# Optimization experiments

Hardware: AMD Instinct MI355X
Metric: run time of the kernel (lower is better)

Reference implementation:

```python
import math
import jax, jax.numpy as jnp
import numpy as np

B, L, D = 2, 2048, 1024
NH = 16
HS = D // NH
BLOCK_SIZE = 2048


def setup_inputs() -> dict:
    key = jax.random.key(0)
    ks = jax.random.split(key, 4)
    x = jax.random.normal(ks[0], (B, L, D), dtype=jnp.float32)
    Wqkv = jax.random.normal(ks[1], (D, 3 * D), dtype=jnp.float32) * 0.02
    bqkv = jnp.zeros((3 * D,), dtype=jnp.float32)
    Wproj = jax.random.normal(ks[2], (D, D), dtype=jnp.float32) * 0.02
    bproj = jnp.zeros((D,), dtype=jnp.float32)
    Er = jax.random.normal(ks[3], (BLOCK_SIZE, HS), dtype=jnp.float32)
    return {"x": x, "Wqkv": Wqkv, "bqkv": bqkv, "Wproj": Wproj, "bproj": bproj, "Er": Er}


def _skew(QEr):
    # QEr: [B, nh, L, L]  (Music Transformer skew trick)
    b, nh, nr, nc = QEr.shape
    padded = jnp.pad(QEr, ((0, 0), (0, 0), (0, 0), (1, 0)))  # [B, nh, nr, nc+1]
    reshaped = padded.reshape(b, nh, nc + 1, nr)
    return reshaped[:, :, 1:, :]  # [B, nh, nr, nc]


def reference(x, Wqkv, bqkv, Wproj, bproj, Er):
    b, l, d = x.shape
    qkv = x @ Wqkv + bqkv  # [B, L, 3D]
    q, k, v = jnp.split(qkv, 3, axis=2)
    q = q.reshape(b, l, NH, HS).transpose(0, 2, 1, 3)  # [B, nh, L, hs]
    k = k.reshape(b, l, NH, HS).transpose(0, 2, 1, 3)
    v = v.reshape(b, l, NH, HS).transpose(0, 2, 1, 3)

    start = BLOCK_SIZE - l
    Er_t = Er[start:, :].T  # [hs, L]
    QEr = jnp.einsum('bhld,dm->bhlm', q, Er_t)  # [B, nh, L, L]
    Srel = _skew(QEr)

    QK_t = jnp.einsum('bhld,bhmd->bhlm', q, k)
    scale = 1.0 / math.sqrt(HS)
    att = (QK_t + Srel) * scale
    causal = jnp.tril(jnp.ones((l, l), dtype=bool))
    att = jnp.where(causal[None, None, :, :], att, jnp.float32(-jnp.inf))
    att = jax.nn.softmax(att, axis=-1)
    y = jnp.einsum('bhlm,bhmd->bhld', att, v)
    y = y.transpose(0, 2, 1, 3).reshape(b, l, d)
    return y @ Wproj + bproj
```

## Files before the change

kernel.cpp:

```cpp
#include <hip/hip_runtime.h>
#include <stdint.h>

#define BB 2
#define LL 2048
#define DD 1024
#define NHH 16
#define HSS 64

typedef __bf16 bf16x8 __attribute__((ext_vector_type(8)));
typedef float f32x4 __attribute__((ext_vector_type(4)));

__device__ __forceinline__ bf16x8 load8(const float* p) {
  float4 f0 = *(const float4*)p;
  float4 f1 = *(const float4*)(p + 4);
  bf16x8 v;
  v[0] = (__bf16)f0.x; v[1] = (__bf16)f0.y; v[2] = (__bf16)f0.z; v[3] = (__bf16)f0.w;
  v[4] = (__bf16)f1.x; v[5] = (__bf16)f1.y; v[6] = (__bf16)f1.z; v[7] = (__bf16)f1.w;
  return v;
}
__device__ __forceinline__ bf16x8 load8(const __bf16* p) {
  return *(const bf16x8*)p;
}

__device__ __forceinline__ void async_ld16(__bf16* lds_uniform_base,
                                           const __bf16* gptr_per_lane) {
  __builtin_amdgcn_global_load_lds(
      (const __attribute__((address_space(1))) void*)gptr_per_lane,
      (__attribute__((address_space(3))) void*)lds_uniform_base, 16, 0, 0);
}

__global__ void prep_k(const float* __restrict__ Wqkv, const float* __restrict__ x,
                       __bf16* __restrict__ WqkvT, __bf16* __restrict__ xb) {
  __shared__ __bf16 tile[32][33];
  int tx = threadIdx.x, ty = threadIdx.y;
  if (blockIdx.z == 1) {
    if (blockIdx.x >= 2048) return;
    int tid = ty * 32 + tx;
    size_t off = ((size_t)blockIdx.x * 256 + tid) * 8;
    *(bf16x8*)&xb[off] = load8(&x[off]);
    return;
  }
  int c0 = (blockIdx.x % 96) * 32, r0 = (blockIdx.x / 96) * 32;
#pragma unroll
  for (int i = ty; i < 32; i += 8)
    tile[i][tx] = (__bf16)Wqkv[(size_t)(r0 + i) * 3072 + c0 + tx];
  __syncthreads();
#pragma unroll
  for (int i = ty; i < 32; i += 8)
    WqkvT[(size_t)(c0 + i) * 1024 + r0 + tx] = tile[tx][i];
}

__global__ void tconv_k(const float* __restrict__ src, __bf16* __restrict__ dst,
                        int R, int C) {
  __shared__ __bf16 tile[32][33];
  int c0 = blockIdx.x * 32, r0 = blockIdx.y * 32;
  int tx = threadIdx.x, ty = threadIdx.y;
#pragma unroll
  for (int i = ty; i < 32; i += 8)
    tile[i][tx] = (__bf16)src[(size_t)(r0 + i) * C + c0 + tx];
  __syncthreads();
#pragma unroll
  for (int i = ty; i < 32; i += 8)
    dst[(size_t)(c0 + i) * R + r0 + tx] = tile[tx][i];
}

__global__ void vtrans_k(const __bf16* __restrict__ src, __bf16* __restrict__ dst) {
  __shared__ __bf16 tile[32][33];
  int bh = blockIdx.z;
  int l0 = blockIdx.x * 32, d0 = blockIdx.y * 32;
  const __bf16* s = src + (size_t)bh * LL * HSS;
  __bf16* d = dst + (size_t)bh * HSS * LL;
  int tx = threadIdx.x, ty = threadIdx.y;
#pragma unroll
  for (int i = ty; i < 32; i += 8)
    tile[i][tx] = s[(size_t)(l0 + i) * HSS + d0 + tx];
  __syncthreads();
#pragma unroll
  for (int i = ty; i < 32; i += 8)
    d[(size_t)(d0 + i) * LL + l0 + tx] = tile[tx][i];
}

template <int NTILE>
__global__ __launch_bounds__(256) void gemm_async_k(
    const __bf16* __restrict__ A, const __bf16* __restrict__ Bt,
    const float* __restrict__ bias, int M, int N, int K, int mode,
    float* __restrict__ out, __bf16* __restrict__ Qo,
    __bf16* __restrict__ Ko, __bf16* __restrict__ Vo) {
  constexpr int NF = NTILE / 32;
  constexpr int BG = NTILE / 64;
  __shared__ __align__(16) __bf16 As[128 * 32];
  __shared__ __align__(16) __bf16 Bs[NTILE * 32];
  int t = threadIdx.x;
  int wave = t >> 6, lane = t & 63, qd = lane >> 4, lr = lane & 15;
  int m0 = blockIdx.y * 128, n0 = blockIdx.x * NTILE;
  int wm = (wave >> 1) * 64, wn = (wave & 1) * (NTILE / 2);
  f32x4 acc[4][NF] = {};
  int srow = lane >> 2, sch = (lane & 3) * 8;

  const __bf16* Ab[2];
  const __bf16* Bb[BG];
#pragma unroll
  for (int c = 0; c < 2; c++)
    Ab[c] = A + (size_t)(m0 + (wave * 2 + c) * 16 + srow) * K + sch;
#pragma unroll
  for (int c = 0; c < BG; c++)
    Bb[c] = Bt + (size_t)(n0 + (wave * BG + c) * 16 + srow) * K + sch;

  for (int k0 = 0; k0 < K; k0 += 32) {
    __syncthreads();
#pragma unroll
    for (int c = 0; c < 2; c++)
      async_ld16(&As[(wave * 2 + c) * 512], Ab[c] + k0);
#pragma unroll
    for (int c = 0; c < BG; c++)
      async_ld16(&Bs[(wave * BG + c) * 512], Bb[c] + k0);
    __syncthreads();
    bf16x8 af[4], bfr[NF];
#pragma unroll
    for (int mt = 0; mt < 4; mt++)
      af[mt] = *(const bf16x8*)&As[(wm + mt * 16 + lr) * 32 + qd * 8];
#pragma unroll
    for (int nt = 0; nt < NF; nt++)
      bfr[nt] = *(const bf16x8*)&Bs[(wn + nt * 16 + lr) * 32 + qd * 8];
#pragma unroll
    for (int mt = 0; mt < 4; mt++)
#pragma unroll
      for (int nt = 0; nt < NF; nt++)
        acc[mt][nt] = __builtin_amdgcn_mfma_f32_16x16x32_bf16(af[mt], bfr[nt],
                                                              acc[mt][nt], 0, 0, 0);
  }
  float bvv[NF];
#pragma unroll
  for (int nt = 0; nt < NF; nt++) bvv[nt] = bias[n0 + wn + nt * 16 + lr];
#pragma unroll
  for (int mt = 0; mt < 4; mt++) {
#pragma unroll
    for (int nt = 0; nt < NF; nt++) {
#pragma unroll
      for (int r = 0; r < 4; r++) {
        int row = m0 + wm + mt * 16 + qd * 4 + r;
        int col = n0 + wn + nt * 16 + lr;
        float v = acc[mt][nt][r] + bvv[nt];
        if (mode == 1) {
          out[(size_t)row * N + col] = v;
        } else {
          __bf16 bb = (__bf16)v;
          int b = row >> 11, l = row & 2047;
          int h = (col >> 6) & 15, d = col & 63;
          __bf16* dst = (col < DD) ? Qo : (col < 2 * DD) ? Ko : Vo;
          dst[(((size_t)(b * NHH + h)) * LL + l) * HSS + d] = bb;
        }
      }
    }
  }
}

__global__ __launch_bounds__(256, 2) void flash_k(
    const __bf16* __restrict__ Qg, const __bf16* __restrict__ Kg,
    const __bf16* __restrict__ Vtg, const float* __restrict__ Erg,
    __bf16* __restrict__ Yg) {
  __shared__ __align__(16) __bf16 Kld[64 * 72];
  __shared__ __align__(16) __bf16 Vld[80 * 72];
  __shared__ __align__(16) __bf16 Erld[128 * 72];
  __shared__ __align__(16) __bf16 Pball[4][16 * 72];

  int bh = blockIdx.y;
  const __bf16* Qh = Qg + (size_t)bh * LL * HSS;
  const __bf16* Kh = Kg + (size_t)bh * LL * HSS;
  const __bf16* Vth = Vtg + (size_t)bh * HSS * LL;
  int b = bh >> 4, h = bh & 15;
  int t = threadIdx.x, wave = t >> 6, lane = t & 63, qd = lane >> 4, lr = lane & 15;
  __bf16* Pb = &Pball[wave][0];
  int cbase = 48 - wave * 16;

  for (int idx = t; idx < 16 * 72; idx += 256) {
    int rr = idx / 72;
    Vld[(64 + rr) * 72 + (idx - rr * 72)] = (rr == 0) ? (__bf16)1.f : (__bf16)0.f;
  }

  int jj = t >> 2, hf = t & 3;
  int er = t >> 1, ec = (t & 1) * 32;

#pragma unroll 1
  for (int pass = 0; pass < 2; pass++) {
    int tile = (pass == 0) ? (int)blockIdx.x : (31 - (int)blockIdx.x);
    int i0 = tile * 64;

    bf16x8 aq[2];
    {
      const __bf16* qrow = Qh + (size_t)(i0 + wave * 16 + lr) * HSS + qd * 8;
      aq[0] = *(const bf16x8*)qrow;
      aq[1] = *(const bf16x8*)(qrow + 32);
    }
    f32x4 oacc[5] = {};

    bf16x8 kr0, kr1, vr0, vr1, ergs[4];
    auto prefetch = [&](int j0) {
      kr0 = *(const bf16x8*)&Kh[(size_t)(j0 + jj) * HSS + hf * 16];
      kr1 = *(const bf16x8*)&Kh[(size_t)(j0 + jj) * HSS + hf * 16 + 8];
      vr0 = *(const bf16x8*)&Vth[(size_t)jj * LL + j0 + hf * 16];
      vr1 = *(const bf16x8*)&Vth[(size_t)jj * LL + j0 + hf * 16 + 8];
      int e = LL - 64 - i0 + j0 + er;
      if (e < LL) {
#pragma unroll
        for (int kx = 0; kx < 4; kx++)
          ergs[kx] = load8(&Erg[(size_t)e * HSS + ec + kx * 8]);
      } else {
        bf16x8 z;
#pragma unroll
        for (int q = 0; q < 8; q++) z[q] = (__bf16)0.f;
#pragma unroll
        for (int kx = 0; kx < 4; kx++) ergs[kx] = z;
      }
    };
    prefetch(0);

    for (int j0 = 0; j0 <= i0; j0 += 64) {
      __syncthreads();
      *(bf16x8*)&Kld[jj * 72 + hf * 16] = kr0;
      *(bf16x8*)&Kld[jj * 72 + hf * 16 + 8] = kr1;
      *(bf16x8*)&Vld[jj * 72 + hf * 16] = vr0;
      *(bf16x8*)&Vld[jj * 72 + hf * 16 + 8] = vr1;
#pragma unroll
      for (int kx = 0; kx < 4; kx++)
        *(bf16x8*)&Erld[er * 72 + ec + kx * 8] = ergs[kx];
      __syncthreads();
      if (j0 + 64 <= i0) prefetch(j0 + 64);

      f32x4 sacc[4] = {};
#pragma unroll
      for (int ct = 0; ct < 4; ct++)
#pragma unroll
        for (int kc = 0; kc < 2; kc++) {
          bf16x8 bk = *(const bf16x8*)&Kld[(ct * 16 + lr) * 72 + kc * 32 + qd * 8];
          sacc[ct] = __builtin_amdgcn_mfma_f32_16x16x32_bf16(aq[kc], bk, sacc[ct], 0, 0, 0);
        }
      f32x4 racc[5] = {};
#pragma unroll
      for (int ct = 0; ct < 5; ct++)
#pragma unroll
        for (int kc = 0; kc < 2; kc++) {
          bf16x8 be = *(const bf16x8*)&Erld[(cbase + ct * 16 + lr) * 72 + kc * 32 + qd * 8];
          racc[ct] = __builtin_amdgcn_mfma_f32_16x16x32_bf16(aq[kc], be, racc[ct], 0, 0, 0);
        }

#pragma unroll
      for (int r = 0; r < 4; r++) {
        int tr = qd * 4 + r;
        int base = 15 - tr + lr;
        int src = qd * 16 + (base & 15);
        int hi = base >> 4;
        float sh[5];
#pragma unroll
        for (int ct = 0; ct < 5; ct++) sh[ct] = __shfl(racc[ct][r], src, 64);
        int gi = i0 + wave * 16 + tr;
#pragma unroll
        for (int ct2 = 0; ct2 < 4; ct2++) {
          float rel = hi ? sh[ct2 + 1] : sh[ct2];
          float s = (sacc[ct2][r] + rel) * 0.125f;
          int gj = j0 + ct2 * 16 + lr;
          float p = (gj <= gi) ? __expf(s) : 0.f;
          Pb[tr * 72 + ct2 * 16 + lr] = (__bf16)p;
        }
      }

      bf16x8 ap0 = *(const bf16x8*)&Pb[lr * 72 + qd * 8];
      bf16x8 ap1 = *(const bf16x8*)&Pb[lr * 72 + 32 + qd * 8];
#pragma unroll
      for (int dt = 0; dt < 5; dt++) {
        bf16x8 bv0 = *(const bf16x8*)&Vld[(dt * 16 + lr) * 72 + qd * 8];
        bf16x8 bv1 = *(const bf16x8*)&Vld[(dt * 16 + lr) * 72 + 32 + qd * 8];
        oacc[dt] = __builtin_amdgcn_mfma_f32_16x16x32_bf16(ap0, bv0, oacc[dt], 0, 0, 0);
        oacc[dt] = __builtin_amdgcn_mfma_f32_16x16x32_bf16(ap1, bv1, oacc[dt], 0, 0, 0);
      }
    }

#pragma unroll
    for (int r = 0; r < 4; r++) {
      float lv = __shfl(oacc[4][r], qd * 16, 64);
      float inv = 1.f / lv;
      int l = i0 + wave * 16 + qd * 4 + r;
#pragma unroll
      for (int dt = 0; dt < 4; dt++) {
        int d = dt * 16 + lr;
        Yg[((size_t)(b * LL) + l) * DD + h * HSS + d] = (__bf16)(oacc[dt][r] * inv);
      }
    }
  }
}

extern "C" void kernel_launch(void* const* d_in, const int* in_sizes, int n_in,
                              void* d_out, int out_size, void* d_ws, size_t ws_size,
                              hipStream_t stream) {
  const float* x = (const float*)d_in[0];
  const float* Wqkv = (const float*)d_in[1];
  const float* bqkv = (const float*)d_in[2];
  const float* Wproj = (const float*)d_in[3];
  const float* bproj = (const float*)d_in[4];
  const float* Er = (const float*)d_in[5];
  float* out = (float*)d_out;

  if (ws_size < 4u * 8388608u) return;

  uint8_t* w = (uint8_t*)d_ws;
  __bf16* Q = (__bf16*)w;  w += (size_t)BB * NHH * LL * HSS * 2;
  __bf16* Kt = (__bf16*)w; w += (size_t)BB * NHH * LL * HSS * 2;
  __bf16* Vt = (__bf16*)w; w += (size_t)BB * NHH * LL * HSS * 2;
  __bf16* Y = (__bf16*)w;  w += (size_t)BB * LL * DD * 2;

  __bf16* xb = Y;
  __bf16* WqkvT = (__bf16*)d_out;
  __bf16* Vtmp = (__bf16*)((uint8_t*)d_out + (size_t)3072 * 1024 * 2);
  __bf16* WprojT = Q;

  prep_k<<<dim3(3072, 1, 2), dim3(32, 8), 0, stream>>>(Wqkv, x, WqkvT, xb);
  gemm_async_k<128><<<dim3(3072 / 128, 4096 / 128), 256, 0, stream>>>(
      xb, WqkvT, bqkv, 4096, 3072, 1024, 0, nullptr, Q, Kt, Vtmp);
  vtrans_k<<<dim3(LL / 32, HSS / 32, BB * NHH), dim3(32, 8), 0, stream>>>(Vtmp, Vt);
  flash_k<<<dim3(16, BB * NHH), 256, 0, stream>>>(Q, Kt, Vt, Er, Y);
  tconv_k<<<dim3(1024 / 32, 1024 / 32), dim3(32, 8), 0, stream>>>(Wproj, WprojT, 1024, 1024);
  gemm_async_k<64><<<dim3(1024 / 64, 4096 / 128), 256, 0, stream>>>(
      Y, WprojT, bproj, 4096, 1024, 1024, 1, out, nullptr, nullptr, nullptr);
}
```

Before: 259.9 us.

## Fuse transposes into GEMMs, pre-convert Er, and split flash tiles per block

The QKV GEMM epilogue now writes V directly in transposed layout, which removes the separate vtrans kernel. The projection GEMM reads fp32 Wproj and transposes it into LDS itself, which removes the tconv kernel. Er is converted to bf16 once in the prep kernel, and flash reads its fragments straight from global memory instead of staging them in LDS. Flash now runs one query tile per block (grid 32x32, largest tiles first, occupancy hint 3) instead of pairing tiles over two passes. This cuts launches and LDS use, but adds strided V stores, an uncoalesced Er gather from global, and a scalar LDS transpose in the projection GEMM.

```diff
diff --git a/kernel.cpp b/kernel.cpp
--- a/kernel.cpp
+++ b/kernel.cpp
@@ -30,16 +30,23 @@
 }
 
 __global__ void prep_k(const float* __restrict__ Wqkv, const float* __restrict__ x,
-                       __bf16* __restrict__ WqkvT, __bf16* __restrict__ xb) {
-  __shared__ __bf16 tile[32][33];
+                       const float* __restrict__ Er, __bf16* __restrict__ WqkvT,
+                       __bf16* __restrict__ xb, __bf16* __restrict__ Erb) {
   int tx = threadIdx.x, ty = threadIdx.y;
+  int tid = ty * 32 + tx;
   if (blockIdx.z == 1) {
     if (blockIdx.x >= 2048) return;
-    int tid = ty * 32 + tx;
     size_t off = ((size_t)blockIdx.x * 256 + tid) * 8;
     *(bf16x8*)&xb[off] = load8(&x[off]);
     return;
   }
+  if (blockIdx.z == 2) {
+    if (blockIdx.x >= 64) return;
+    size_t off = ((size_t)blockIdx.x * 256 + tid) * 8;
+    *(bf16x8*)&Erb[off] = load8(&Er[off]);
+    return;
+  }
+  __shared__ __bf16 tile[32][33];
   int c0 = (blockIdx.x % 96) * 32, r0 = (blockIdx.x / 96) * 32;
 #pragma unroll
   for (int i = ty; i < 32; i += 8)
@@ -50,121 +57,139 @@
     WqkvT[(size_t)(c0 + i) * 1024 + r0 + tx] = tile[tx][i];
 }
 
-__global__ void tconv_k(const float* __restrict__ src, __bf16* __restrict__ dst,
-                        int R, int C) {
-  __shared__ __bf16 tile[32][33];
-  int c0 = blockIdx.x * 32, r0 = blockIdx.y * 32;
-  int tx = threadIdx.x, ty = threadIdx.y;
-#pragma unroll
-  for (int i = ty; i < 32; i += 8)
-    tile[i][tx] = (__bf16)src[(size_t)(r0 + i) * C + c0 + tx];
-  __syncthreads();
-#pragma unroll
-  for (int i = ty; i < 32; i += 8)
-    dst[(size_t)(c0 + i) * R + r0 + tx] = tile[tx][i];
-}
-
-__global__ void vtrans_k(const __bf16* __restrict__ src, __bf16* __restrict__ dst) {
-  __shared__ __bf16 tile[32][33];
-  int bh = blockIdx.z;
-  int l0 = blockIdx.x * 32, d0 = blockIdx.y * 32;
-  const __bf16* s = src + (size_t)bh * LL * HSS;
-  __bf16* d = dst + (size_t)bh * HSS * LL;
-  int tx = threadIdx.x, ty = threadIdx.y;
-#pragma unroll
-  for (int i = ty; i < 32; i += 8)
-    tile[i][tx] = s[(size_t)(l0 + i) * HSS + d0 + tx];
-  __syncthreads();
-#pragma unroll
-  for (int i = ty; i < 32; i += 8)
-    d[(size_t)(d0 + i) * LL + l0 + tx] = tile[tx][i];
-}
-
-template <int NTILE>
-__global__ __launch_bounds__(256) void gemm_async_k(
+__global__ __launch_bounds__(256) void gemm_qkv_k(
     const __bf16* __restrict__ A, const __bf16* __restrict__ Bt,
-    const float* __restrict__ bias, int M, int N, int K, int mode,
-    float* __restrict__ out, __bf16* __restrict__ Qo,
-    __bf16* __restrict__ Ko, __bf16* __restrict__ Vo) {
-  constexpr int NF = NTILE / 32;
-  constexpr int BG = NTILE / 64;
+    const float* __restrict__ bias, __bf16* __restrict__ Qo,
+    __bf16* __restrict__ Ko, __bf16* __restrict__ Vto) {
+  const int K = 1024;
   __shared__ __align__(16) __bf16 As[128 * 32];
-  __shared__ __align__(16) __bf16 Bs[NTILE * 32];
+  __shared__ __align__(16) __bf16 Bs[128 * 32];
   int t = threadIdx.x;
   int wave = t >> 6, lane = t & 63, qd = lane >> 4, lr = lane & 15;
-  int m0 = blockIdx.y * 128, n0 = blockIdx.x * NTILE;
-  int wm = (wave >> 1) * 64, wn = (wave & 1) * (NTILE / 2);
-  f32x4 acc[4][NF] = {};
+  int m0 = blockIdx.y * 128, n0 = blockIdx.x * 128;
+  int wm = (wave >> 1) * 64, wn = (wave & 1) * 64;
+  f32x4 acc[4][4] = {};
   int srow = lane >> 2, sch = (lane & 3) * 8;
-
   const __bf16* Ab[2];
-  const __bf16* Bb[BG];
-#pragma unroll
-  for (int c = 0; c < 2; c++)
+  const __bf16* Bb[2];
+#pragma unroll
+  for (int c = 0; c < 2; c++) {
     Ab[c] = A + (size_t)(m0 + (wave * 2 + c) * 16 + srow) * K + sch;
-#pragma unroll
-  for (int c = 0; c < BG; c++)
-    Bb[c] = Bt + (size_t)(n0 + (wave * BG + c) * 16 + srow) * K + sch;
-
+    Bb[c] = Bt + (size_t)(n0 + (wave * 2 + c) * 16 + srow) * K + sch;
+  }
   for (int k0 = 0; k0 < K; k0 += 32) {
     __syncthreads();
 #pragma unroll
-    for (int c = 0; c < 2; c++)
+    for (int c = 0; c < 2; c++) {
       async_ld16(&As[(wave * 2 + c) * 512], Ab[c] + k0);
-#pragma unroll
-    for (int c = 0; c < BG; c++)
-      async_ld16(&Bs[(wave * BG + c) * 512], Bb[c] + k0);
-    __syncthreads();
-    bf16x8 af[4], bfr[NF];
+      async_ld16(&Bs[(wave * 2 + c) * 512], Bb[c] + k0);
+    }
+    __syncthreads();
+    bf16x8 af[4], bfr[4];
 #pragma unroll
     for (int mt = 0; mt < 4; mt++)
       af[mt] = *(const bf16x8*)&As[(wm + mt * 16 + lr) * 32 + qd * 8];
 #pragma unroll
-    for (int nt = 0; nt < NF; nt++)
+    for (int nt = 0; nt < 4; nt++)
       bfr[nt] = *(const bf16x8*)&Bs[(wn + nt * 16 + lr) * 32 + qd * 8];
 #pragma unroll
     for (int mt = 0; mt < 4; mt++)
 #pragma unroll
-      for (int nt = 0; nt < NF; nt++)
+      for (int nt = 0; nt < 4; nt++)
         acc[mt][nt] = __builtin_amdgcn_mfma_f32_16x16x32_bf16(af[mt], bfr[nt],
                                                               acc[mt][nt], 0, 0, 0);
   }
-  float bvv[NF];
-#pragma unroll
-  for (int nt = 0; nt < NF; nt++) bvv[nt] = bias[n0 + wn + nt * 16 + lr];
-#pragma unroll
-  for (int mt = 0; mt < 4; mt++) {
-#pragma unroll
-    for (int nt = 0; nt < NF; nt++) {
+  float bvv[4];
+#pragma unroll
+  for (int nt = 0; nt < 4; nt++) bvv[nt] = bias[n0 + wn + nt * 16 + lr];
+#pragma unroll
+  for (int mt = 0; mt < 4; mt++)
+#pragma unroll
+    for (int nt = 0; nt < 4; nt++)
 #pragma unroll
       for (int r = 0; r < 4; r++) {
         int row = m0 + wm + mt * 16 + qd * 4 + r;
         int col = n0 + wn + nt * 16 + lr;
-        float v = acc[mt][nt][r] + bvv[nt];
-        if (mode == 1) {
-          out[(size_t)row * N + col] = v;
+        __bf16 bb = (__bf16)(acc[mt][nt][r] + bvv[nt]);
+        int b = row >> 11, l = row & 2047;
+        int h = (col >> 6) & 15, d = col & 63;
+        if (col < DD) {
+          Qo[(((size_t)(b * NHH + h)) * LL + l) * HSS + d] = bb;
+        } else if (col < 2 * DD) {
+          Ko[(((size_t)(b * NHH + h)) * LL + l) * HSS + d] = bb;
         } else {
-          __bf16 bb = (__bf16)v;
-          int b = row >> 11, l = row & 2047;
-          int h = (col >> 6) & 15, d = col & 63;
-          __bf16* dst = (col < DD) ? Qo : (col < 2 * DD) ? Ko : Vo;
-          dst[(((size_t)(b * NHH + h)) * LL + l) * HSS + d] = bb;
+          Vto[(((size_t)(b * NHH + h)) * HSS + d) * LL + l] = bb;
         }
       }
-    }
-  }
-}
-
-__global__ __launch_bounds__(256, 2) void flash_k(
+}
+
+__global__ __launch_bounds__(256) void gemm_proj_k(
+    const __bf16* __restrict__ A, const float* __restrict__ Bg,
+    const float* __restrict__ bias, float* __restrict__ out) {
+  const int K = 1024, N = 1024;
+  __shared__ __align__(16) __bf16 As[128 * 32];
+  __shared__ __align__(16) __bf16 Bs[64 * 40];
+  int t = threadIdx.x;
+  int wave = t >> 6, lane = t & 63, qd = lane >> 4, lr = lane & 15;
+  int m0 = blockIdx.y * 128, n0 = blockIdx.x * 64;
+  int wm = (wave >> 1) * 64, wn = (wave & 1) * 32;
+  f32x4 acc[4][2] = {};
+  int srow = lane >> 2, sch = (lane & 3) * 8;
+  const __bf16* Ab[2];
+#pragma unroll
+  for (int c = 0; c < 2; c++)
+    Ab[c] = A + (size_t)(m0 + (wave * 2 + c) * 16 + srow) * K + sch;
+  int kk = t >> 3, nn = (t & 7) * 8;
+  const float* Bp = Bg + (size_t)kk * N + n0 + nn;
+
+  for (int k0 = 0; k0 < K; k0 += 32) {
+    __syncthreads();
+#pragma unroll
+    for (int c = 0; c < 2; c++)
+      async_ld16(&As[(wave * 2 + c) * 512], Ab[c] + k0);
+    bf16x8 bv = load8(Bp + (size_t)k0 * N);
+#pragma unroll
+    for (int j = 0; j < 8; j++) Bs[(nn + j) * 40 + kk] = bv[j];
+    __syncthreads();
+    bf16x8 af[4], bfr[2];
+#pragma unroll
+    for (int mt = 0; mt < 4; mt++)
+      af[mt] = *(const bf16x8*)&As[(wm + mt * 16 + lr) * 32 + qd * 8];
+#pragma unroll
+    for (int nt = 0; nt < 2; nt++)
+      bfr[nt] = *(const bf16x8*)&Bs[(wn + nt * 16 + lr) * 40 + qd * 8];
+#pragma unroll
+    for (int mt = 0; mt < 4; mt++)
+#pragma unroll
+      for (int nt = 0; nt < 2; nt++)
+        acc[mt][nt] = __builtin_amdgcn_mfma_f32_16x16x32_bf16(af[mt], bfr[nt],
+                                                              acc[mt][nt], 0, 0, 0);
+  }
+  float bvv[2];
+#pragma unroll
+  for (int nt = 0; nt < 2; nt++) bvv[nt] = bias[n0 + wn + nt * 16 + lr];
+#pragma unroll
+  for (int mt = 0; mt < 4; mt++)
+#pragma unroll
+    for (int nt = 0; nt < 2; nt++)
+#pragma unroll
+      for (int r = 0; r < 4; r++) {
+        int row = m0 + wm + mt * 16 + qd * 4 + r;
+        int col = n0 + wn + nt * 16 + lr;
+        out[(size_t)row * N + col] = acc[mt][nt][r] + bvv[nt];
+      }
+}
+
+__global__ __launch_bounds__(256, 3) void flash_k(
     const __bf16* __restrict__ Qg, const __bf16* __restrict__ Kg,
-    const __bf16* __restrict__ Vtg, const float* __restrict__ Erg,
+    const __bf16* __restrict__ Vtg, const __bf16* __restrict__ Erb,
     __bf16* __restrict__ Yg) {
   __shared__ __align__(16) __bf16 Kld[64 * 72];
   __shared__ __align__(16) __bf16 Vld[80 * 72];
-  __shared__ __align__(16) __bf16 Erld[128 * 72];
   __shared__ __align__(16) __bf16 Pball[4][16 * 72];
 
-  int bh = blockIdx.y;
+  int bh = blockIdx.x;
+  int i0 = (31 - (int)blockIdx.y) * 64;
   const __bf16* Qh = Qg + (size_t)bh * LL * HSS;
   const __bf16* Kh = Kg + (size_t)bh * LL * HSS;
   const __bf16* Vth = Vtg + (size_t)bh * HSS * LL;
@@ -179,112 +204,100 @@
   }
 
   int jj = t >> 2, hf = t & 3;
-  int er = t >> 1, ec = (t & 1) * 32;
-
-#pragma unroll 1
-  for (int pass = 0; pass < 2; pass++) {
-    int tile = (pass == 0) ? (int)blockIdx.x : (31 - (int)blockIdx.x);
-    int i0 = tile * 64;
-
-    bf16x8 aq[2];
-    {
-      const __bf16* qrow = Qh + (size_t)(i0 + wave * 16 + lr) * HSS + qd * 8;
-      aq[0] = *(const bf16x8*)qrow;
-      aq[1] = *(const bf16x8*)(qrow + 32);
-    }
-    f32x4 oacc[5] = {};
-
-    bf16x8 kr0, kr1, vr0, vr1, ergs[4];
-    auto prefetch = [&](int j0) {
-      kr0 = *(const bf16x8*)&Kh[(size_t)(j0 + jj) * HSS + hf * 16];
-      kr1 = *(const bf16x8*)&Kh[(size_t)(j0 + jj) * HSS + hf * 16 + 8];
-      vr0 = *(const bf16x8*)&Vth[(size_t)jj * LL + j0 + hf * 16];
-      vr1 = *(const bf16x8*)&Vth[(size_t)jj * LL + j0 + hf * 16 + 8];
-      int e = LL - 64 - i0 + j0 + er;
-      if (e < LL) {
-#pragma unroll
-        for (int kx = 0; kx < 4; kx++)
-          ergs[kx] = load8(&Erg[(size_t)e * HSS + ec + kx * 8]);
-      } else {
-        bf16x8 z;
-#pragma unroll
-        for (int q = 0; q < 8; q++) z[q] = (__bf16)0.f;
-#pragma unroll
-        for (int kx = 0; kx < 4; kx++) ergs[kx] = z;
+
+  bf16x8 aq[2];
+  {
+    const __bf16* qrow = Qh + (size_t)(i0 + wave * 16 + lr) * HSS + qd * 8;
+    aq[0] = *(const bf16x8*)qrow;
+    aq[1] = *(const bf16x8*)(qrow + 32);
+  }
+  f32x4 oacc[5] = {};
+
+  bf16x8 kr0, kr1, vr0, vr1;
+  auto prefetch = [&](int j0) {
+    kr0 = *(const bf16x8*)&Kh[(size_t)(j0 + jj) * HSS + hf * 16];
+    kr1 = *(const bf16x8*)&Kh[(size_t)(j0 + jj) * HSS + hf * 16 + 8];
+    vr0 = *(const bf16x8*)&Vth[(size_t)jj * LL + j0 + hf * 16];
+    vr1 = *(const bf16x8*)&Vth[(size_t)jj * LL + j0 + hf * 16 + 8];
+  };
+  prefetch(0);
+
+  for (int j0 = 0; j0 <= i0; j0 += 64) {
+    __syncthreads();
+    *(bf16x8*)&Kld[jj * 72 + hf * 16] = kr0;
+    *(bf16x8*)&Kld[jj * 72 + hf * 16 + 8] = kr1;
+    *(bf16x8*)&Vld[jj * 72 + hf * 16] = vr0;
+    *(bf16x8*)&Vld[jj * 72 + hf * 16 + 8] = vr1;
+    __syncthreads();
+    if (j0 + 64 <= i0) prefetch(j0 + 64);
+
+    bf16x8 ef[5][2];
+    int ebase = LL - 64 - i0 + j0 + cbase;
+#pragma unroll
+    for (int ct = 0; ct < 5; ct++) {
+      int e = ebase + ct * 16 + lr;
+      e = (e < LL) ? e : (LL - 1);
+#pragma unroll
+      for (int kc = 0; kc < 2; kc++)
+        ef[ct][kc] = *(const bf16x8*)&Erb[(size_t)e * HSS + kc * 32 + qd * 8];
+    }
+
+    f32x4 sacc[4] = {};
+#pragma unroll
+    for (int ct = 0; ct < 4; ct++)
+#pragma unroll
+      for (int kc = 0; kc < 2; kc++) {
+        bf16x8 bk = *(const bf16x8*)&Kld[(ct * 16 + lr) * 72 + kc * 32 + qd * 8];
+        sacc[ct] = __builtin_amdgcn_mfma_f32_16x16x32_bf16(aq[kc], bk, sacc[ct], 0, 0, 0);
       }
-    };
-    prefetch(0);
-
-    for (int j0 = 0; j0 <= i0; j0 += 64) {
-      __syncthreads();
-      *(bf16x8*)&Kld[jj * 72 + hf * 16] = kr0;
-      *(bf16x8*)&Kld[jj * 72 + hf * 16 + 8] = kr1;
-      *(bf16x8*)&Vld[jj * 72 + hf * 16] = vr0;
-      *(bf16x8*)&Vld[jj * 72 + hf * 16 + 8] = vr1;
-#pragma unroll
-      for (int kx = 0; kx < 4; kx++)
-        *(bf16x8*)&Erld[er * 72 + ec + kx * 8] = ergs[kx];
-      __syncthreads();
-      if (j0 + 64 <= i0) prefetch(j0 + 64);
-
-      f32x4 sacc[4] = {};
-#pragma unroll
-      for (int ct = 0; ct < 4; ct++)
-#pragma unroll
-        for (int kc = 0; kc < 2; kc++) {
-          bf16x8 bk = *(const bf16x8*)&Kld[(ct * 16 + lr) * 72 + kc * 32 + qd * 8];
-          sacc[ct] = __builtin_amdgcn_mfma_f32_16x16x32_bf16(aq[kc], bk, sacc[ct], 0, 0, 0);
-        }
-      f32x4 racc[5] = {};
-#pragma unroll
-      for (int ct = 0; ct < 5; ct++)
-#pragma unroll
-        for (int kc = 0; kc < 2; kc++) {
-          bf16x8 be = *(const bf16x8*)&Erld[(cbase + ct * 16 + lr) * 72 + kc * 32 + qd * 8];
-          racc[ct] = __builtin_amdgcn_mfma_f32_16x16x32_bf16(aq[kc], be, racc[ct], 0, 0, 0);
-        }
-
-#pragma unroll
-      for (int r = 0; r < 4; r++) {
-        int tr = qd * 4 + r;
-        int base = 15 - tr + lr;
-        int src = qd * 16 + (base & 15);
-        int hi = base >> 4;
-        float sh[5];
-#pragma unroll
-        for (int ct = 0; ct < 5; ct++) sh[ct] = __shfl(racc[ct][r], src, 64);
-        int gi = i0 + wave * 16 + tr;
-#pragma unroll
-        for (int ct2 = 0; ct2 < 4; ct2++) {
-          float rel = hi ? sh[ct2 + 1] : sh[ct2];
-          float s = (sacc[ct2][r] + rel) * 0.125f;
-          int gj = j0 + ct2 * 16 + lr;
-          float p = (gj <= gi) ? __expf(s) : 0.f;
-          Pb[tr * 72 + ct2 * 16 + lr] = (__bf16)p;
-        }
+    f32x4 racc[5] = {};
+#pragma unroll
+    for (int ct = 0; ct < 5; ct++)
+#pragma unroll
+      for (int kc = 0; kc < 2; kc++)
+        racc[ct] = __builtin_amdgcn_mfma_f32_16x16x32_bf16(aq[kc], ef[ct][kc],
+                                                           racc[ct], 0, 0, 0);
+
+#pragma unroll
+    for (int r = 0; r < 4; r++) {
+      int tr = qd * 4 + r;
+      int base = 15 - tr + lr;
+      int src = qd * 16 + (base & 15);
+      int hi = base >> 4;
+      float sh[5];
+#pragma unroll
+      for (int ct = 0; ct < 5; ct++) sh[ct] = __shfl(racc[ct][r], src, 64);
+      int gi = i0 + wave * 16 + tr;
+#pragma unroll
+      for (int ct2 = 0; ct2 < 4; ct2++) {
+        float rel = hi ? sh[ct2 + 1] : sh[ct2];
+        float s = (sacc[ct2][r] + rel) * 0.125f;
+        int gj = j0 + ct2 * 16 + lr;
+        float p = (gj <= gi) ? __expf(s) : 0.f;
+        Pb[tr * 72 + ct2 * 16 + lr] = (__bf16)p;
       }
-
-      bf16x8 ap0 = *(const bf16x8*)&Pb[lr * 72 + qd * 8];
-      bf16x8 ap1 = *(const bf16x8*)&Pb[lr * 72 + 32 + qd * 8];
-#pragma unroll
-      for (int dt = 0; dt < 5; dt++) {
-        bf16x8 bv0 = *(const bf16x8*)&Vld[(dt * 16 + lr) * 72 + qd * 8];
-        bf16x8 bv1 = *(const bf16x8*)&Vld[(dt * 16 + lr) * 72 + 32 + qd * 8];
-        oacc[dt] = __builtin_amdgcn_mfma_f32_16x16x32_bf16(ap0, bv0, oacc[dt], 0, 0, 0);
-        oacc[dt] = __builtin_amdgcn_mfma_f32_16x16x32_bf16(ap1, bv1, oacc[dt], 0, 0, 0);
-      }
-    }
-
-#pragma unroll
-    for (int r = 0; r < 4; r++) {
-      float lv = __shfl(oacc[4][r], qd * 16, 64);
-      float inv = 1.f / lv;
-      int l = i0 + wave * 16 + qd * 4 + r;
-#pragma unroll
-      for (int dt = 0; dt < 4; dt++) {
-        int d = dt * 16 + lr;
-        Yg[((size_t)(b * LL) + l) * DD + h * HSS + d] = (__bf16)(oacc[dt][r] * inv);
-      }
+    }
+
+    bf16x8 ap0 = *(const bf16x8*)&Pb[lr * 72 + qd * 8];
+    bf16x8 ap1 = *(const bf16x8*)&Pb[lr * 72 + 32 + qd * 8];
+#pragma unroll
+    for (int dt = 0; dt < 5; dt++) {
+      bf16x8 bv0 = *(const bf16x8*)&Vld[(dt * 16 + lr) * 72 + qd * 8];
+      bf16x8 bv1 = *(const bf16x8*)&Vld[(dt * 16 + lr) * 72 + 32 + qd * 8];
+      oacc[dt] = __builtin_amdgcn_mfma_f32_16x16x32_bf16(ap0, bv0, oacc[dt], 0, 0, 0);
+      oacc[dt] = __builtin_amdgcn_mfma_f32_16x16x32_bf16(ap1, bv1, oacc[dt], 0, 0, 0);
+    }
+  }
+
+#pragma unroll
+  for (int r = 0; r < 4; r++) {
+    float lv = __shfl(oacc[4][r], qd * 16, 64);
+    float inv = 1.f / lv;
+    int l = i0 + wave * 16 + qd * 4 + r;
+#pragma unroll
+    for (int dt = 0; dt < 4; dt++) {
+      int d = dt * 16 + lr;
+      Yg[((size_t)(b * LL) + l) * DD + h * HSS + d] = (__bf16)(oacc[dt][r] * inv);
     }
   }
 }
@@ -308,17 +321,13 @@
   __bf16* Vt = (__bf16*)w; w += (size_t)BB * NHH * LL * HSS * 2;
   __bf16* Y = (__bf16*)w;  w += (size_t)BB * LL * DD * 2;
 
-  __bf16* xb = Y;
   __bf16* WqkvT = (__bf16*)d_out;
-  __bf16* Vtmp = (__bf16*)((uint8_t*)d_out + (size_t)3072 * 1024 * 2);
-  __bf16* WprojT = Q;
-
-  prep_k<<<dim3(3072, 1, 2), dim3(32, 8), 0, stream>>>(Wqkv, x, WqkvT, xb);
-  gemm_async_k<128><<<dim3(3072 / 128, 4096 / 128), 256, 0, stream>>>(
-      xb, WqkvT, bqkv, 4096, 3072, 1024, 0, nullptr, Q, Kt, Vtmp);
-  vtrans_k<<<dim3(LL / 32, HSS / 32, BB * NHH), dim3(32, 8), 0, stream>>>(Vtmp, Vt);
-  flash_k<<<dim3(16, BB * NHH), 256, 0, stream>>>(Q, Kt, Vt, Er, Y);
-  tconv_k<<<dim3(1024 / 32, 1024 / 32), dim3(32, 8), 0, stream>>>(Wproj, WprojT, 1024, 1024);
-  gemm_async_k<64><<<dim3(1024 / 64, 4096 / 128), 256, 0, stream>>>(
-      Y, WprojT, bproj, 4096, 1024, 1024, 1, out, nullptr, nullptr, nullptr);
-}
+  __bf16* xb = (__bf16*)((uint8_t*)d_out + (size_t)3072 * 1024 * 2);
+  __bf16* Erb = (__bf16*)((uint8_t*)d_out + (size_t)3072 * 1024 * 2 + (size_t)4096 * 1024 * 2);
+
+  prep_k<<<dim3(3072, 1, 3), dim3(32, 8), 0, stream>>>(Wqkv, x, Er, WqkvT, xb, Erb);
+  gemm_qkv_k<<<dim3(3072 / 128, 4096 / 128), 256, 0, stream>>>(
+      xb, WqkvT, bqkv, Q, Kt, Vt);
+  flash_k<<<dim3(BB * NHH, 32), 256, 0, stream>>>(Q, Kt, Vt, Erb, Y);
+  gemm_proj_k<<<dim3(1024 / 64, 4096 / 128), 256, 0, stream>>>(Y, Wproj, bproj, out);
+}
```

Measured after the change: 263.8 us. No clear change (+1.5%).
